# Kernel tuning notes

Hardware: AMD Instinct MI355X
Metric: run time of the kernel (lower is better)

Reference implementation:

```python
import jax, jax.numpy as jnp
import numpy as np

# NTU RGB+D 25-joint skeleton edges (1-based)
NTU_EDGES = [(1,2),(2,21),(3,21),(4,3),(5,21),(6,5),(7,6),(8,7),(9,21),(10,9),
             (11,10),(12,11),(13,1),(14,13),(15,14),(16,15),(17,1),(18,17),
             (19,18),(20,19),(22,23),(23,8),(24,25),(25,12)]
NUM_SCALES = 13
NUM_POINT = 25


def build_A_powers(num_scales=NUM_SCALES, v=NUM_POINT):
    # MS-G3D disentangled multi-scale aggregation: exact-k-hop adjacencies, each
    # with self loops, symmetrically normalized, stacked along dim 0 -> (K*V, V).
    A = np.zeros((v, v))
    for i, j in NTU_EDGES:
        A[i - 1, j - 1] = 1.0
        A[j - 1, i - 1] = 1.0
    I = np.eye(v)
    mats = []
    for k in range(num_scales):
        if k == 0:
            Ak = I.copy()
        else:
            Ak = np.minimum(np.linalg.matrix_power(A + I, k), 1) \
               - np.minimum(np.linalg.matrix_power(A + I, k - 1), 1)
            Ak = Ak + I  # with_self=True
        d = Ak.sum(-1)
        dinv = np.where(d > 0, d ** -0.5, 0.0)
        mats.append((dinv[:, None] * Ak) * dinv[None, :])
    return np.concatenate(mats, 0).astype(np.float32)


def batchnorm(x, g, b, axes, ch_axis, eps=1e-5):
    # torch BatchNorm in training mode: biased batch stats + affine
    mean = jnp.mean(x, axes, keepdims=True)
    var = jnp.mean((x - mean) ** 2, axes, keepdims=True)
    shape = [1] * x.ndim
    shape[ch_axis] = -1
    return (x - mean) * jax.lax.rsqrt(var + eps) * g.reshape(shape) + b.reshape(shape)


def ms_gcn(x, A_powers, A_res, W, b, g, beta, num_scales):
    # x: (N, C, T, V); A: (K*V, V)
    A = A_powers + A_res
    support = jnp.einsum('vu,nctu->nctv', A, x)            # (N, C, T, K*V)
    N, C, T, KV = support.shape
    V = KV // num_scales
    support = support.reshape(N, C, T, num_scales, V).transpose(0, 3, 1, 2, 4)
    support = support.reshape(N, num_scales * C, T, V)     # (N, K*C, T, V)
    out = jnp.einsum('oc,nctv->notv', W, support) + b[None, :, None, None]  # 1x1 conv
    out = batchnorm(out, g, beta, (0, 2, 3), 1)
    return jax.nn.relu(out)


def lstm(x, Wih, Whh, bih, bhh):
    # single-layer batch_first LSTM, zero initial state; torch gate order i,f,g,o
    B = x.shape[0]
    H = Whh.shape[1]
    xp = jnp.einsum('bsd,hd->bsh', x, Wih) + bih + bhh     # precompute input proj

    def step(carry, xt):
        h, c = carry
        gates = xt + h @ Whh.T
        i, f, g, o = jnp.split(gates, 4, axis=-1)
        c = jax.nn.sigmoid(f) * c + jax.nn.sigmoid(i) * jnp.tanh(g)
        h = jax.nn.sigmoid(o) * jnp.tanh(c)
        return (h, c), h

    init = (jnp.zeros((B, H), x.dtype), jnp.zeros((B, H), x.dtype))
    _, ys = jax.lax.scan(step, init, jnp.swapaxes(xp, 0, 1))
    return jnp.swapaxes(ys, 0, 1)                          # (B, S, H)


def logsig_rnn(x, n_segments, Wih, Whh, bih, bhh):
    # x: (B, T, d). Depth-2 log-signature per time segment + segment start point,
    # concatenated and fed to an LSTM (Logsig-RNN layer).
    B, T, d = x.shape
    t_vec = np.array([int(round(float(v))) for v in np.linspace(1, T, n_segments + 1)])
    starts = t_vec[:-1] - 1
    ends = t_vec[1:] - 1
    L = int((ends - starts).max()) + 1
    # pad segments to fixed length by repeating the last point (zero increments)
    idx = np.minimum(starts[:, None] + np.arange(L)[None, :], ends[:, None])  # (S, L)
    pts = x[:, idx, :]                                     # (B, S, L, d)
    rel = pts - pts[:, :, :1, :]
    inc = rel[:, :, -1, :]                                 # level-1: total increment
    dx = pts[:, :, 1:, :] - pts[:, :, :-1, :]
    Mm = jnp.einsum('bsli,bslj->bsij', rel[:, :, :-1, :], dx)
    iu, ju = np.triu_indices(d, k=1)
    levy = 0.5 * (Mm[:, :, iu, ju] - Mm[:, :, ju, iu])     # level-2 (Lyndon basis)
    feats = jnp.concatenate([x[:, starts, :], inc, levy], axis=-1)
    return lstm(feats, Wih, Whh, bih, bhh)


def setup_inputs() -> dict:
    key = jax.random.key(0)
    ks = iter(jax.random.split(key, 16))
    N, C, T, V, M = 2, 3, 100, 25, 2
    c1, c2, num_class, K = 96, 192, 60, NUM_SCALES

    def randn(shape, scale):
        return jax.random.normal(next(ks), shape, jnp.float32) * scale

    ls1 = c1 + c1 * (c1 - 1) // 2     # 4656
    ls2 = c2 + c2 * (c2 - 1) // 2     # 18528
    in1 = c1 + ls1                    # 4752
    in2 = c2 + ls2                    # 18720
    Ap = jnp.asarray(build_A_powers())
    return {
        'x': jax.random.normal(next(ks), (N, C, T, V, M), jnp.float32),
        'length': jax.random.randint(next(ks), (N,), 0, T),
        'data_bn_g': jnp.ones((M * V * C,)), 'data_bn_b': jnp.zeros((M * V * C,)),
        'A_powers1': Ap,
        'A_res1': jax.random.uniform(next(ks), Ap.shape, jnp.float32, -1e-6, 1e-6),
        'W1': randn((c1, K * C), (K * C) ** -0.5), 'b1': jnp.zeros((c1,)),
        'bn1_g': jnp.ones((c1,)), 'bn1_b': jnp.zeros((c1,)),
        'Wih1': randn((4 * c1, in1), in1 ** -0.5), 'Whh1': randn((4 * c1, c1), c1 ** -0.5),
        'bih1': jnp.zeros((4 * c1,)), 'bhh1': jnp.zeros((4 * c1,)),
        'bnseg1_g': jnp.ones((50,)), 'bnseg1_b': jnp.zeros((50,)),
        'A_powers2': Ap,
        'A_res2': jax.random.uniform(next(ks), Ap.shape, jnp.float32, -1e-6, 1e-6),
        'W2': randn((c2, K * c1), (K * c1) ** -0.5), 'b2': jnp.zeros((c2,)),
        'bn2_g': jnp.ones((c2,)), 'bn2_b': jnp.zeros((c2,)),
        'Wih2': randn((4 * c2, in2), in2 ** -0.5), 'Whh2': randn((4 * c2, c2), c2 ** -0.5),
        'bih2': jnp.zeros((4 * c2,)), 'bhh2': jnp.zeros((4 * c2,)),
        'bnseg2_g': jnp.ones((30,)), 'bnseg2_b': jnp.zeros((30,)),
        'fcW': randn((num_class, c2), c2 ** -0.5), 'fcb': jnp.zeros((num_class,)),
    }


def reference(x, length, data_bn_g, data_bn_b, A_powers1, A_res1, W1, b1, bn1_g, bn1_b,
              Wih1, Whh1, bih1, bhh1, bnseg1_g, bnseg1_b, A_powers2, A_res2, W2, b2,
              bn2_g, bn2_b, Wih2, Whh2, bih2, bhh2, bnseg2_g, bnseg2_b, fcW, fcb):
    # `length` is accepted but unused, as in the original forward.
    N, C, T, V, M = x.shape
    K = A_powers1.shape[0] // V
    c1, c2 = W1.shape[0], W2.shape[0]
    S1, S2 = 50, 30

    h = x.transpose(0, 4, 3, 1, 2).reshape(N, M * V * C, T)
    h = batchnorm(h, data_bn_g, data_bn_b, (0, 2), 1)
    h = h.reshape(N * M, V, C, T).transpose(0, 2, 3, 1)            # (NM, C, T, V)

    h = jax.nn.relu(ms_gcn(h, A_powers1, A_res1, W1, b1, bn1_g, bn1_b, K))
    h = h.transpose(0, 3, 2, 1).reshape(N * M * V, T, c1)
    h = logsig_rnn(h, S1, Wih1, Whh1, bih1, bhh1)                  # (NMV, S1, c1)
    h = batchnorm(h, bnseg1_g, bnseg1_b, (0, 2), 1)
    h = h.reshape(N * M, V, S1, c1).transpose(0, 3, 2, 1)          # (NM, c1, S1, V)

    h = jax.nn.relu(ms_gcn(h, A_powers2, A_res2, W2, b2, bn2_g, bn2_b, K))
    h = h.transpose(0, 3, 2, 1).reshape(N * M * V, S1, c2)
    h = logsig_rnn(h, S2, Wih2, Whh2, bih2, bhh2)                  # (NMV, S2, c2)
    h = batchnorm(h, bnseg2_g, bnseg2_b, (0, 2), 1)
    h = h.reshape(N * M, V, S2, c2).transpose(0, 3, 2, 1)          # (NM, c2, S2, V)

    pooled = h.reshape(N, M, c2, -1).mean(axis=3).mean(axis=1)     # (N, c2)
    return pooled @ fcW.T + fcb
```

## Files before the change

kernel.cpp:

```cpp
#include <hip/hip_runtime.h>
#include <cmath>
#include <cstdint>
#include <cstddef>

typedef unsigned short bf16_t;
typedef __attribute__((ext_vector_type(8))) short short8;
typedef __attribute__((ext_vector_type(4))) float floatx4;
typedef __attribute__((ext_vector_type(2))) _Float16 half2_t;

__device__ __forceinline__ float bf2f(bf16_t b){
  unsigned int u = ((unsigned int)b) << 16;
  return __uint_as_float(u);
}
__device__ __forceinline__ bf16_t f2bf(float f){
  unsigned int u = __float_as_uint(f);
  unsigned int r = (u + 0x7fffu + ((u >> 16) & 1u)) >> 16;
  return (bf16_t)r;
}
__device__ __forceinline__ unsigned int f2bf2(float a, float b){
  return (unsigned int)f2bf(a) | ((unsigned int)f2bf(b) << 16);
}
__device__ __forceinline__ float sigf(float x){ return 1.0f / (1.0f + expf(-x)); }

__device__ __forceinline__ float dot2(half2_t a, half2_t b, float c){
#if __has_builtin(__builtin_amdgcn_fdot2)
  return __builtin_amdgcn_fdot2(a, b, c, false);
#else
  return c + (float)a.x * (float)b.x + (float)a.y * (float)b.y;
#endif
}

__device__ __forceinline__ void gload_lds16(const bf16_t* g, bf16_t* lds){
  __builtin_amdgcn_global_load_lds(
      (const __attribute__((address_space(1))) unsigned int*)g,
      (__attribute__((address_space(3))) unsigned int*)lds, 16, 0, 0);
}

__device__ __forceinline__ void barrier_raw(){
  asm volatile("s_barrier" ::: "memory");
}

__device__ __forceinline__ int xcd_chunk_swizzle(int orig, int nwg){
  int q = nwg >> 3, r = nwg & 7;
  int xcd = orig & 7, idx = orig >> 3;
  return (xcd < r ? xcd * (q + 1) : r * (q + 1) + (xcd - r) * q) + idx;
}

__global__ void prep_misc(const float* __restrict__ a1, const float* __restrict__ r1, float* __restrict__ o1,
                          const float* __restrict__ a2, const float* __restrict__ r2, float* __restrict__ o2,
                          const float* __restrict__ bi1, const float* __restrict__ bh1, float* __restrict__ ob1,
                          const float* __restrict__ bi2, const float* __restrict__ bh2, float* __restrict__ ob2,
                          const float* __restrict__ Whh1, half2_t* __restrict__ Wp1,
                          const float* __restrict__ Whh2, half2_t* __restrict__ Wp2,
                          unsigned short* __restrict__ lut1, unsigned short* __restrict__ lut2,
                          float* __restrict__ stats, bf16_t* __restrict__ A2mat){
  int i = blockIdx.x * blockDim.x + threadIdx.x;
  if (i < 8125){ o1[i] = a1[i] + r1[i]; o2[i] = a2[i] + r2[i]; }
  if (i < 384) ob1[i] = bi1[i] + bh1[i];
  if (i < 768) ob2[i] = bi2[i] + bh2[i];
  if (i < 736) stats[i] = 0.f;
  if (i < 18432){
    int t = i % 384, j2 = i / 384;
    half2_t w; w.x = (_Float16)Whh1[(size_t)t * 96 + 2 * j2];
    w.y = (_Float16)Whh1[(size_t)t * 96 + 2 * j2 + 1];
    Wp1[i] = w;
  }
  if (i < 73728){
    int t = i % 768, j2 = i / 768;
    half2_t w; w.x = (_Float16)Whh2[(size_t)t * 192 + 2 * j2];
    w.y = (_Float16)Whh2[(size_t)t * 192 + 2 * j2 + 1];
    Wp2[i] = w;
  }
  if (i < 4560){
    int d = 96, p = i;
    int r = (int)(((2.0 * d - 1.0) - sqrt((2.0 * d - 1.0) * (2.0 * d - 1.0) - 8.0 * (double)p)) * 0.5);
    if (r < 0) r = 0;
    while (r + 1 <= d - 2 && (r + 1) * (d - 1) - ((r + 1) * r) / 2 <= p) ++r;
    while (r > 0 && r * (d - 1) - (r * (r - 1)) / 2 > p) --r;
    int jj = p - (r * (d - 1) - (r * (r - 1)) / 2);
    lut1[p] = (unsigned short)((r << 8) | (r + 1 + jj));
  }
  if (i < 18336){
    int d = 192, p = i;
    int r = (int)(((2.0 * d - 1.0) - sqrt((2.0 * d - 1.0) * (2.0 * d - 1.0) - 8.0 * (double)p)) * 0.5);
    if (r < 0) r = 0;
    while (r + 1 <= d - 2 && (r + 1) * (d - 1) - ((r + 1) * r) / 2 <= p) ++r;
    while (r > 0 && r * (d - 1) - (r * (r - 1)) / 2 > p) --r;
    int jj = p - (r * (d - 1) - (r * (r - 1)) / 2);
    lut2[p] = (unsigned short)((r << 8) | (r + 1 + jj));
  }
  if (i < 160000){
    int row = i >> 5, col = 1248 + (i & 31);
    A2mat[(size_t)row * 1280 + col] = 0;
  }
}

__device__ __forceinline__ void f2bf_seg(const float* in, bf16_t* out, int Kin, int Kout, int li){
  int ko8 = Kout >> 3;
  int r = li / ko8, k8 = (li % ko8) << 3;
  uint4 u;
  if (k8 + 8 <= Kin){
    const float4* p = reinterpret_cast<const float4*>(in + (size_t)r * Kin + k8);
    float4 x0 = p[0], x1 = p[1];
    u.x = f2bf2(x0.x, x0.y); u.y = f2bf2(x0.z, x0.w);
    u.z = f2bf2(x1.x, x1.y); u.w = f2bf2(x1.z, x1.w);
  } else {
    u.x = u.y = u.z = u.w = 0u;
  }
  *reinterpret_cast<uint4*>(out + (size_t)r * Kout + k8) = u;
}

__global__ void f2bf_pad8_3(const float* __restrict__ in1, bf16_t* __restrict__ out1, int Kin1, int Kout1, int c1,
                            const float* __restrict__ in2, bf16_t* __restrict__ out2, int Kin2, int Kout2, int c2,
                            const float* __restrict__ in3, bf16_t* __restrict__ out3, int Kin3, int Kout3, int c3){
  int idx = blockIdx.x * blockDim.x + threadIdx.x;
  if (idx < c1){ f2bf_seg(in1, out1, Kin1, Kout1, idx); return; }
  idx -= c1;
  if (idx < c2){ f2bf_seg(in2, out2, Kin2, Kout2, idx); return; }
  idx -= c2;
  if (idx < c3) f2bf_seg(in3, out3, Kin3, Kout3, idx);
}

__global__ void data_bn_kernel(const float* __restrict__ x, const float* __restrict__ g,
                               const float* __restrict__ bb, float* __restrict__ h1,
                               int N, int C, int T, int V, int M){
  int ch = blockIdx.x;
  int m = ch / (V * C);
  int v = (ch / C) % V;
  int c = ch % C;
  int tid = threadIdx.x;
  int cnt = N * T;
  float s = 0.f, s2 = 0.f;
  for (int i = tid; i < cnt; i += 64){
    int n = i / T, t = i % T;
    float val = x[(((size_t)(n * C + c) * T + t) * V + v) * M + m];
    s += val; s2 += val * val;
  }
  for (int off = 32; off; off >>= 1){ s += __shfl_down(s, off); s2 += __shfl_down(s2, off); }
  s = __shfl(s, 0); s2 = __shfl(s2, 0);
  float mean = s / cnt;
  float rstd = rsqrtf(s2 / cnt - mean * mean + 1e-5f);
  float gg = g[ch], bo = bb[ch];
  for (int i = tid; i < cnt; i += 64){
    int n = i / T, t = i % T;
    float val = x[(((size_t)(n * C + c) * T + t) * V + v) * M + m];
    float y = (val - mean) * rstd * gg + bo;
    h1[((size_t)((n * M + m) * C + c) * T + t) * V + v] = y;
  }
}

__global__ __launch_bounds__(256)
void gcn1_fused(const float* __restrict__ A, const float* __restrict__ h1,
                const float* __restrict__ W1, const float* __restrict__ b1,
                float* __restrict__ y1, float* __restrict__ ssum, float* __restrict__ ssq, int T){
  __shared__ float h[3][25];
  __shared__ float sup[3][325];
  __shared__ float lsum[96], lsq[96];
  int blk = blockIdx.x;
  int nm = blk / T, t = blk % T;
  int tid = threadIdx.x;
  if (tid < 75){
    int c = tid / 25, v = tid % 25;
    h[c][v] = h1[((size_t)(nm * 3 + c) * T + t) * 25 + v];
  }
  if (tid < 96){ lsum[tid] = 0.f; lsq[tid] = 0.f; }
  __syncthreads();
  for (int w = tid; w < 975; w += 256){
    int c = w / 325, ww = w % 325;
    const float* ar = A + ww * 25;
    float acc = 0.f;
    #pragma unroll
    for (int u = 0; u < 25; ++u) acc += ar[u] * h[c][u];
    sup[c][ww] = acc;
  }
  __syncthreads();
  for (int o2 = tid; o2 < 2400; o2 += 256){
    int v = o2 / 96, o = o2 % 96;
    float acc = b1[o];
    #pragma unroll
    for (int k = 0; k < 13; ++k)
      #pragma unroll
      for (int c = 0; c < 3; ++c)
        acc += W1[o * 39 + k * 3 + c] * sup[c][k * 25 + v];
    y1[((size_t)blk * 25 + v) * 96 + o] = acc;
    atomicAdd(&lsum[o], acc);
    atomicAdd(&lsq[o], acc * acc);
  }
  __syncthreads();
  if (tid < 96){ atomicAdd(&ssum[tid], lsum[tid]); atomicAdd(&ssq[tid], lsq[tid]); }
}

struct SegTable { int st[50]; int en[50]; };

__global__ void feats_bn_kernel(const float* __restrict__ ymat, const float* __restrict__ sum,
                                const float* __restrict__ sumsq, const float* __restrict__ g,
                                const float* __restrict__ bb, bf16_t* __restrict__ feats,
                                SegTable segs, const unsigned int* __restrict__ lut32,
                                int T, int d, int S, int L, int pairs, int rowlenP, int R){
  __shared__ float pts[4][192];
  int bs = blockIdx.x;
  int b = bs / S, s = bs % S;
  int nm = b / 25, v = b % 25;
  int st = segs.st[s], en = segs.en[s];
  int nt = blockDim.x, tid = threadIdx.x;
  for (int l = 0; l < L; ++l){
    int t = st + l; if (t > en) t = en;
    const float* yrow = ymat + ((size_t)(nm * T + t) * 25 + v) * d;
    for (int i = tid; i < d; i += nt){
      float mean = sum[i] / R;
      float rstd = rsqrtf(sumsq[i] / R - mean * mean + 1e-5f);
      pts[l][i] = fmaxf((yrow[i] - mean) * rstd * g[i] + bb[i], 0.f);
    }
  }
  __syncthreads();
  unsigned int* frow32 = reinterpret_cast<unsigned int*>(feats + (size_t)bs * rowlenP);
  int d2 = d >> 1;
  for (int i2 = tid; i2 < d2; i2 += nt){
    int i = 2 * i2;
    frow32[i2]      = f2bf2(pts[0][i], pts[0][i + 1]);
    frow32[d2 + i2] = f2bf2(pts[L - 1][i] - pts[0][i], pts[L - 1][i + 1] - pts[0][i + 1]);
  }
  int rowlen2 = (2 * d + pairs) >> 1, rowlenP2 = rowlenP >> 1;
  for (int i = tid + rowlen2; i < rowlenP2; i += nt) frow32[i] = 0;
  int Lm2 = L - 2;
  unsigned int* lrow32 = frow32 + d;
  int pairs2 = pairs >> 1;
  for (int p2 = tid; p2 < pairs2; p2 += nt){
    unsigned int ee = lut32[p2];
    int i0 = (ee >> 8) & 255, j0 = ee & 255;
    int i1 = ee >> 24, j1 = (ee >> 16) & 255;
    float acc0 = 0.f, acc1 = 0.f;
    for (int l = 1; l <= Lm2; ++l){
      float ri = pts[l][i0] - pts[0][i0], rj = pts[l][j0] - pts[0][j0];
      float di = pts[l + 1][i0] - pts[l][i0], dj = pts[l + 1][j0] - pts[l][j0];
      acc0 += ri * dj - rj * di;
      float ri1 = pts[l][i1] - pts[0][i1], rj1 = pts[l][j1] - pts[0][j1];
      float di1 = pts[l + 1][i1] - pts[l][i1], dj1 = pts[l + 1][j1] - pts[l][j1];
      acc1 += ri1 * dj1 - rj1 * di1;
    }
    lrow32[p2] = f2bf2(0.5f * acc0, 0.5f * acc1);
  }
}

__global__ __launch_bounds__(256)
void gemm_mfma_nt_split(const bf16_t* __restrict__ A, const bf16_t* __restrict__ B,
                        float* __restrict__ P, int M, int N, int K,
                        int GX, int GY, int GZ){
  __shared__ bf16_t As[128 * 64];
  __shared__ bf16_t Bs[128 * 64];
  const int nwg = GX * GY * GZ;
  const int wg = xcd_chunk_swizzle(blockIdx.x, nwg);
  const int bxi = wg % GX, byi = (wg / GX) % GY, bzi = wg / (GX * GY);
  const int tid = threadIdx.x;
  const int lane = tid & 63, wv = tid >> 6;
  const int bm = bxi * 128, bn = byi * 128;
  const int wr = (wv >> 1) * 64, wc = (wv & 1) * 64;
  const int m_l = lane & 15, q = lane >> 4;

  const int ksteps = K >> 6;
  const int Z = GZ, z = bzi;
  const int per = (ksteps + Z - 1) / Z;
  const int ks0 = z * per;
  const int ks1 = (ks0 + per < ksteps) ? ks0 + per : ksteps;

  const int rlane = lane >> 3;
  const int slane = lane & 7;
  const int colc = (slane ^ rlane) * 8;
  const bf16_t* gA[4]; const bf16_t* gB[4];
  bf16_t* lA[4]; bf16_t* lB[4];
  #pragma unroll
  for (int it = 0; it < 4; ++it){
    int c = it * 4 + wv;
    int rowA = bm + c * 8 + rlane; if (rowA > M - 1) rowA = M - 1;
    int rowB = bn + c * 8 + rlane; if (rowB > N - 1) rowB = N - 1;
    gA[it] = A + (size_t)rowA * K + colc;
    gB[it] = B + (size_t)rowB * K + colc;
    lA[it] = &As[c * 512];
    lB[it] = &Bs[c * 512];
  }
  const int sxor = m_l & 7;

  floatx4 acc[4][4] = {};
  for (int ks = ks0; ks < ks1; ++ks){
    int k0 = ks << 6;
    __syncthreads();
    #pragma unroll
    for (int it = 0; it < 4; ++it){
      gload_lds16(gA[it] + k0, lA[it]);
      gload_lds16(gB[it] + k0, lB[it]);
    }
    __syncthreads();
    #pragma unroll
    for (int half = 0; half < 2; ++half){
      const int scol = ((half * 4 + q) ^ sxor) * 8;
      short8 af[4], bfr[4];
      #pragma unroll
      for (int i = 0; i < 4; ++i){
        af[i]  = *reinterpret_cast<const short8*>(&As[(wr + i * 16 + m_l) * 64 + scol]);
        bfr[i] = *reinterpret_cast<const short8*>(&Bs[(wc + i * 16 + m_l) * 64 + scol]);
      }
      #pragma unroll
      for (int mi = 0; mi < 4; ++mi)
        #pragma unroll
        for (int ni = 0; ni < 4; ++ni)
          acc[mi][ni] = __builtin_amdgcn_mfma_f32_16x16x32_bf16(af[mi], bfr[ni], acc[mi][ni], 0, 0, 0);
    }
  }

  float* Pz = P + (size_t)z * M * N;
  #pragma unroll
  for (int mi = 0; mi < 4; ++mi){
    int row0 = bm + wr + mi * 16 + q * 4;
    #pragma unroll
    for (int r = 0; r < 4; ++r){
      int row = row0 + r;
      if (row < M){
        #pragma unroll
        for (int ni = 0; ni < 4; ++ni){
          int col = bn + wc + ni * 16 + m_l;
          if (col < N) Pz[(size_t)row * N + col] = acc[mi][ni][r];
        }
      }
    }
  }
}

#define VMC4 asm volatile("s_waitcnt vmcnt(4)" ::: "memory")
#define VMC0 asm volatile("s_waitcnt vmcnt(0)" ::: "memory")
#define STG_A8(NB, KH, OFF) { gload_lds16(pA0 + (OFF) + (KH) * 32, dA0 + (NB) * 16384 + (KH) * 8192); \
                              gload_lds16(pA1 + (OFF) + (KH) * 32, dA1 + (NB) * 16384 + (KH) * 8192); }
#define STG_B8(NB, KH, OFF) { gload_lds16(pB0 + (OFF) + (KH) * 32, dB0 + (NB) * 16384 + (KH) * 8192); \
                              gload_lds16(pB1 + (OFF) + (KH) * 32, dB1 + (NB) * 16384 + (KH) * 8192); }
#define PH8(BUF, KH, MIB, LOADB, STAGE_BLOCK, WAIT_BLOCK) { \
    const bf16_t* ab_ = As + (BUF) * 16384 + (KH) * 8192 + sA + (MIB) * 512; \
    _Pragma("unroll") \
    for (int i_ = 0; i_ < 4; ++i_) af[i_] = *reinterpret_cast<const short8*>(ab_ + i_ * 512); \
    if (LOADB){ \
      const bf16_t* bb_ = Bs + (BUF) * 16384 + (KH) * 8192 + sB; \
      _Pragma("unroll") \
      for (int i_ = 0; i_ < 4; ++i_) bfr[i_] = *reinterpret_cast<const short8*>(bb_ + i_ * 512); \
    } \
    STAGE_BLOCK; \
    WAIT_BLOCK; \
    barrier_raw(); \
    __builtin_amdgcn_s_setprio(1); \
    _Pragma("unroll") \
    for (int mi_ = 0; mi_ < 4; ++mi_) \
      _Pragma("unroll") \
      for (int ni_ = 0; ni_ < 4; ++ni_) \
        acc[(MIB) + mi_][ni_] = __builtin_amdgcn_mfma_f32_16x16x32_bf16(af[mi_], bfr[ni_], acc[(MIB) + mi_][ni_], 0, 0, 0); \
    __builtin_amdgcn_s_setprio(0); \
  }

__global__ __launch_bounds__(512, 2)
void gemm_mfma_nt_8ph(const bf16_t* __restrict__ A, const bf16_t* __restrict__ B,
                      float* __restrict__ P, int M, int N, int K,
                      int GX, int GY, int GZ){
  __shared__ bf16_t As[32768];
  __shared__ bf16_t Bs[32768];
  const int nwg = GX * GY * GZ;
  const int wg = xcd_chunk_swizzle(blockIdx.x, nwg);
  const int bxi = wg % GX, byi = (wg / GX) % GY, bzi = wg / (GX * GY);
  const int tid = threadIdx.x;
  const int lane = tid & 63, wv = tid >> 6;
  const int wm = wv >> 2, wn = wv & 3;
  const int m_l = lane & 15, q = lane >> 4;
  const int bm = bxi * 256, bn = byi * 256;

  const int ksteps = K >> 6;
  const int z = bzi, Z = GZ;
  const int per = (ksteps + Z - 1) / Z;
  const int ks0 = z * per;
  int ks1 = ks0 + per; if (ks1 > ksteps) ks1 = ksteps;
  if (ks0 >= ks1) return;

  const int rlane = lane >> 2, slane = lane & 3;
  const int cg = slane ^ ((rlane >> 1) & 3);
  int rr0 = wv * 16 + rlane, rr1 = (8 + wv) * 16 + rlane;
  int ra0 = bm + rr0; if (ra0 > M - 1) ra0 = M - 1;
  int ra1 = bm + rr1; if (ra1 > M - 1) ra1 = M - 1;
  int rb0 = bn + rr0; if (rb0 > N - 1) rb0 = N - 1;
  int rb1 = bn + rr1; if (rb1 > N - 1) rb1 = N - 1;
  const bf16_t* pA0 = A + (size_t)ra0 * K + cg * 8 + ks0 * 64;
  const bf16_t* pA1 = A + (size_t)ra1 * K + cg * 8 + ks0 * 64;
  const bf16_t* pB0 = B + (size_t)rb0 * K + cg * 8 + ks0 * 64;
  const bf16_t* pB1 = B + (size_t)rb1 * K + cg * 8 + ks0 * 64;
  bf16_t* dA0 = As + wv * 512;
  bf16_t* dA1 = As + (8 + wv) * 512;
  bf16_t* dB0 = Bs + wv * 512;
  bf16_t* dB1 = Bs + (8 + wv) * 512;

  const int sA = (wm * 128 + m_l) * 32 + ((q ^ ((m_l >> 1) & 3)) * 8);
  const int sB = (wn * 64 + m_l) * 32 + ((q ^ ((m_l >> 1) & 3)) * 8);

  short8 af[4], bfr[4];
  floatx4 acc[8][4] = {};

  STG_A8(0, 0, 0); STG_B8(0, 0, 0); STG_A8(0, 1, 0); STG_B8(0, 1, 0);
  VMC4;
  barrier_raw();

  int buf = 0;
  for (int t = ks0; t < ks1 - 1; ++t){
    const int nb = buf ^ 1;
    PH8(buf, 0, 0, true,  STG_A8(nb, 0, 64), ((void)0));
    PH8(buf, 0, 4, false, STG_B8(nb, 0, 64), VMC4);
    PH8(buf, 1, 0, true,  STG_A8(nb, 1, 64), ((void)0));
    PH8(buf, 1, 4, false, STG_B8(nb, 1, 64), VMC4);
    pA0 += 64; pA1 += 64; pB0 += 64; pB1 += 64;
    buf = nb;
  }
  PH8(buf, 0, 0, true,  ((void)0), ((void)0));
  PH8(buf, 0, 4, false, ((void)0), VMC0);
  PH8(buf, 1, 0, true,  ((void)0), ((void)0));
  PH8(buf, 1, 4, false, ((void)0), ((void)0));

  float* Pz = P + (size_t)z * M * N;
  #pragma unroll
  for (int mi = 0; mi < 8; ++mi){
    int row0 = bm + wm * 128 + mi * 16 + q * 4;
    #pragma unroll
    for (int r = 0; r < 4; ++r){
      int row = row0 + r;
      if (row < M){
        #pragma unroll
        for (int ni = 0; ni < 4; ++ni){
          int col = bn + wn * 64 + ni * 16 + m_l;
          if (col < N) Pz[(size_t)row * N + col] = acc[mi][ni][r];
        }
      }
    }
  }
}

__global__ __launch_bounds__(256)
void reduce_split_bias_stats(const float* __restrict__ P, const float* __restrict__ bias,
                             float* __restrict__ out, float* __restrict__ ssum, float* __restrict__ ssq,
                             int MN, int N, int Z){
  __shared__ float lsum[192], lsq[192];
  int tid = threadIdx.x;
  if (tid < 192){ lsum[tid] = 0.f; lsq[tid] = 0.f; }
  __syncthreads();
  int i4 = (blockIdx.x * blockDim.x + tid) * 4;
  if (i4 < MN){
    const float4 bv = *reinterpret_cast<const float4*>(bias + (i4 % N));
    float4 s = bv;
    for (int z = 0; z < Z; ++z){
      const float4 p = *reinterpret_cast<const float4*>(P + (size_t)z * MN + i4);
      s.x += p.x; s.y += p.y; s.z += p.z; s.w += p.w;
    }
    *reinterpret_cast<float4*>(out + i4) = s;
    int c0 = i4 % N;
    atomicAdd(&lsum[c0],     s.x); atomicAdd(&lsq[c0],     s.x * s.x);
    atomicAdd(&lsum[c0 + 1], s.y); atomicAdd(&lsq[c0 + 1], s.y * s.y);
    atomicAdd(&lsum[c0 + 2], s.z); atomicAdd(&lsq[c0 + 2], s.z * s.z);
    atomicAdd(&lsum[c0 + 3], s.w); atomicAdd(&lsq[c0 + 3], s.w * s.w);
  }
  __syncthreads();
  if (tid < 192){ atomicAdd(&ssum[tid], lsum[tid]); atomicAdd(&ssq[tid], lsq[tid]); }
}

template <int H2C, int BLK, int Z>
__global__ __launch_bounds__(BLK)
void lstm_kernel(const float* __restrict__ P, const float* __restrict__ bias,
                 const half2_t* __restrict__ Wp, float* __restrict__ out,
                 float* __restrict__ ssum, float* __restrict__ ssq,
                 int S, int MN){
  constexpr int H = 2 * H2C;
  constexpr int H4 = 4 * H;
  __shared__ _Float16 __attribute__((aligned(16))) hsh[H];
  __shared__ float gv[H4];
  __shared__ float ra[BLK / 64], rb[BLK / 64];
  const int b = blockIdx.x, t = threadIdx.x;
  const int lane = t & 63, wid = t >> 6;
  half2_t w[H2C];
  const half2_t* wp = Wp + t;
  #pragma unroll
  for (int j2 = 0; j2 < H2C; ++j2) w[j2] = wp[(size_t)j2 * H4];
  float cc = 0.f;
  if (t < H) hsh[t] = (_Float16)0.f;
  const float bval = bias[t];
  const size_t base = (size_t)b * S * H4 + t;
  float pv0[Z], pv1[Z];
  #pragma unroll
  for (int z = 0; z < Z; ++z) pv0[z] = P[(size_t)z * MN + base];
  #pragma unroll
  for (int z = 0; z < Z; ++z) pv1[z] = P[(size_t)z * MN + base + H4];
  __syncthreads();
  const half2_t* hp = reinterpret_cast<const half2_t*>(hsh);
  for (int s = 0; s < S; ++s){
    float pvn[Z];
    if (s + 2 < S){
      size_t o2 = base + (size_t)(s + 2) * H4;
      #pragma unroll
      for (int z = 0; z < Z; ++z) pvn[z] = P[(size_t)z * MN + o2];
    }
    float a0 = bval, a1 = 0.f, a2 = 0.f, a3 = 0.f;
    float a4 = 0.f, a5 = 0.f, a6 = 0.f, a7 = 0.f;
    #pragma unroll
    for (int z = 0; z < Z; ++z) a0 += pv0[z];
    #pragma unroll
    for (int j2 = 0; j2 < H2C; j2 += 8){
      a0 = dot2(w[j2],     hp[j2],     a0);
      a1 = dot2(w[j2 + 1], hp[j2 + 1], a1);
      a2 = dot2(w[j2 + 2], hp[j2 + 2], a2);
      a3 = dot2(w[j2 + 3], hp[j2 + 3], a3);
      a4 = dot2(w[j2 + 4], hp[j2 + 4], a4);
      a5 = dot2(w[j2 + 5], hp[j2 + 5], a5);
      a6 = dot2(w[j2 + 6], hp[j2 + 6], a6);
      a7 = dot2(w[j2 + 7], hp[j2 + 7], a7);
    }
    gv[t] = ((a0 + a1) + (a2 + a3)) + ((a4 + a5) + (a6 + a7));
    __syncthreads();
    float gvv = 0.f;
    if (t < H){
      float ig = sigf(gv[t]);
      float fg = sigf(gv[H + t]);
      float gg = tanhf(gv[2 * H + t]);
      float og = sigf(gv[3 * H + t]);
      cc = fg * cc + ig * gg;
      float hh = og * tanhf(cc);
      hsh[t] = (_Float16)hh;
      out[((size_t)b * S + s) * H + t] = hh;
      gvv = hh;
    }
    float q1 = gvv, q2 = gvv * gvv;
    for (int off2 = 32; off2; off2 >>= 1){ q1 += __shfl_down(q1, off2); q2 += __shfl_down(q2, off2); }
    if (lane == 0){ ra[wid] = q1; rb[wid] = q2; }
    __syncthreads();
    if (t == 0){
      float sa = 0.f, sb = 0.f;
      #pragma unroll
      for (int ww = 0; ww < BLK / 64; ++ww){ sa += ra[ww]; sb += rb[ww]; }
      atomicAdd(&ssum[s], sa);
      atomicAdd(&ssq[s], sb);
    }
    #pragma unroll
    for (int z = 0; z < Z; ++z){ pv0[z] = pv1[z]; pv1[z] = pvn[z]; }
  }
}

__global__ void support2_bn(const float* __restrict__ A, const float* __restrict__ lout,
                            const float* __restrict__ ssum, const float* __restrict__ ssq,
                            const float* __restrict__ g, const float* __restrict__ bb,
                            bf16_t* __restrict__ A2mat, int S, int cnt){
  int idx = blockIdx.x * blockDim.x + threadIdx.x;
  int total = 4 * S * 25 * 13 * 96;
  if (idx >= total) return;
  int c = idx % 96;
  int k = (idx / 96) % 13;
  int v = (idx / (96 * 13)) % 25;
  int rs = idx / (96 * 13 * 25);
  int s = rs % S, nm = rs / S;
  float mean = ssum[s] / cnt;
  float rstd = rsqrtf(ssq[s] / cnt - mean * mean + 1e-5f);
  float scale = rstd * g[s];
  float shift = bb[s] - mean * scale;
  const float* ar = A + (k * 25 + v) * 25;
  float acc = 0.f;
  #pragma unroll
  for (int u = 0; u < 25; ++u){
    float raw = lout[((size_t)(nm * 25 + u) * S + s) * 96 + c];
    acc += ar[u] * (raw * scale + shift);
  }
  A2mat[((size_t)rs * 25 + v) * 1280 + k * 96 + c] = f2bf(acc);
}

__global__ void pool_kernel(const float* __restrict__ lout2, const float* __restrict__ sum,
                            const float* __restrict__ sumsq, const float* __restrict__ g,
                            const float* __restrict__ bb, float* __restrict__ pooled,
                            int S, int H, int scnt){
  int n = blockIdx.x / H;
  int o = blockIdx.x % H;
  float acc = 0.f;
  int cnt = 2 * 25 * S;
  for (int i = threadIdx.x; i < cnt; i += 64){
    int m = i / (25 * S);
    int r = i % (25 * S);
    int v = r / S;
    int s = r % S;
    int b = (n * 2 + m) * 25 + v;
    float val = lout2[((size_t)b * S + s) * H + o];
    float mean = sum[s] / scnt;
    float rstd = rsqrtf(sumsq[s] / scnt - mean * mean + 1e-5f);
    val = (val - mean) * rstd * g[s] + bb[s];
    acc += val;
  }
  for (int off = 32; off; off >>= 1) acc += __shfl_down(acc, off);
  if (threadIdx.x == 0) pooled[n * H + o] = acc / cnt;
}

__global__ void fc_kernel(const float* __restrict__ pooled, const float* __restrict__ fcW,
                          const float* __restrict__ fcb, float* __restrict__ outp){
  int idx = blockIdx.x * blockDim.x + threadIdx.x;
  if (idx >= 120) return;
  int n = idx / 60, cls = idx % 60;
  float acc = fcb[cls];
  for (int o = 0; o < 192; ++o) acc += pooled[n * 192 + o] * fcW[cls * 192 + o];
  outp[idx] = acc;
}

static void make_segs(int T, int S, SegTable& tab, int& L){
  double step = (double)(T - 1) / (double)S;
  long long tv[51];
  for (int i = 0; i <= S; ++i){
    double v = 1.0 + step * (double)i;
    tv[i] = llrint(v);
  }
  L = 0;
  for (int s = 0; s < S; ++s){
    tab.st[s] = (int)tv[s] - 1;
    tab.en[s] = (int)tv[s + 1] - 1;
    int len = tab.en[s] - tab.st[s] + 1;
    if (len > L) L = len;
  }
  for (int s = S; s < 50; ++s){ tab.st[s] = 0; tab.en[s] = 0; }
  if (L > 4) L = 4;
}

extern "C" void kernel_launch(void* const* d_in, const int* in_sizes, int n_in,
                              void* d_out, int out_size, void* d_ws, size_t ws_size,
                              hipStream_t stream){
  const float* x         = (const float*)d_in[0];
  const float* data_bn_g = (const float*)d_in[2];
  const float* data_bn_b = (const float*)d_in[3];
  const float* A_powers1 = (const float*)d_in[4];
  const float* A_res1    = (const float*)d_in[5];
  const float* W1        = (const float*)d_in[6];
  const float* b1        = (const float*)d_in[7];
  const float* bn1_g     = (const float*)d_in[8];
  const float* bn1_b     = (const float*)d_in[9];
  const float* Wih1      = (const float*)d_in[10];
  const float* Whh1      = (const float*)d_in[11];
  const float* bih1      = (const float*)d_in[12];
  const float* bhh1      = (const float*)d_in[13];
  const float* bnseg1_g  = (const float*)d_in[14];
  const float* bnseg1_b  = (const float*)d_in[15];
  const float* A_powers2 = (const float*)d_in[16];
  const float* A_res2    = (const float*)d_in[17];
  const float* W2        = (const float*)d_in[18];
  const float* b2        = (const float*)d_in[19];
  const float* bn2_g     = (const float*)d_in[20];
  const float* bn2_b     = (const float*)d_in[21];
  const float* Wih2      = (const float*)d_in[22];
  const float* Whh2      = (const float*)d_in[23];
  const float* bih2      = (const float*)d_in[24];
  const float* bhh2      = (const float*)d_in[25];
  const float* bnseg2_g  = (const float*)d_in[26];
  const float* bnseg2_b  = (const float*)d_in[27];
  const float* fcW       = (const float*)d_in[28];
  const float* fcb       = (const float*)d_in[29];
  float* out = (float*)d_out;

  const int N = 2, C = 3, T = 100, V = 25, M = 2, NM = 4;
  const int C1 = 96, C2 = 192;
  const int S1 = 50, S2 = 30;
  const int B = 100;
  const int IN1 = 4752, IN2 = 18720;
  const int IN1P = 4800, IN2P = 18752;
  const int P1 = 4560, P2 = 18336;
  const int KG2 = 1248, KG2P = 1280;
  const int Z1 = 5, Z2 = 7, ZG = 4;

  size_t off = 0;
  char* base = (char*)d_ws;
  auto alloc = [&](size_t nbytes) -> void* {
    off = (off + 255) & ~(size_t)255;
    void* p = base + off;
    off += nbytes;
    return p;
  };
  float* A1full = (float*)alloc(325 * 25 * 4);
  float* A2full = (float*)alloc(325 * 25 * 4);
  float* h1     = (float*)alloc((size_t)NM * C * T * V * 4);
  float* y1mat  = (float*)alloc((size_t)NM * T * V * C1 * 4);
  float* stats  = (float*)alloc(736 * 4);
  float* st1a = stats, *st1b = stats + 96;
  float* sg1a = stats + 192, *sg1b = stats + 242;
  float* st2a = stats + 292, *st2b = stats + 484;
  float* sg2a = stats + 676, *sg2b = stats + 706;
  float* l1out  = (float*)alloc((size_t)B * S1 * C1 * 4);
  bf16_t* A2mat = (bf16_t*)alloc((size_t)NM * S1 * V * KG2P * 2);
  float* y2mat  = (float*)alloc((size_t)NM * S1 * V * C2 * 4);
  float* l2out  = (float*)alloc((size_t)B * S2 * C2 * 4);
  float* pooled = (float*)alloc(2 * C2 * 4);
  float* bias1  = (float*)alloc(4 * C1 * 4);
  float* bias2  = (float*)alloc(4 * C2 * 4);
  half2_t* Wp1  = (half2_t*)alloc((size_t)(C1 / 2) * 4 * C1 * 4);
  half2_t* Wp2  = (half2_t*)alloc((size_t)(C2 / 2) * 4 * C2 * 4);
  bf16_t* Wih1b = (bf16_t*)alloc((size_t)4 * C1 * IN1P * 2);
  bf16_t* Wih2b = (bf16_t*)alloc((size_t)4 * C2 * IN2P * 2);
  bf16_t* W2b   = (bf16_t*)alloc((size_t)C2 * KG2P * 2);
  unsigned short* lut1 = (unsigned short*)alloc((size_t)P1 * 2);
  unsigned short* lut2 = (unsigned short*)alloc((size_t)P2 * 2);
  size_t pmax = (size_t)Z2 * 3000 * 768;
  {
    size_t p1s = (size_t)Z1 * 5000 * 384; if (p1s > pmax) pmax = p1s;
    size_t pgs = (size_t)ZG * 5000 * 192; if (pgs > pmax) pmax = pgs;
  }
  float* Pbuf = (float*)alloc(pmax * 4);
  bf16_t* feats = (bf16_t*)alloc((size_t)B * S2 * IN2P * 2);
  (void)ws_size; (void)in_sizes; (void)n_in; (void)out_size;

  prep_misc<<<625, 256, 0, stream>>>(A_powers1, A_res1, A1full, A_powers2, A_res2, A2full,
                                     bih1, bhh1, bias1, bih2, bhh2, bias2,
                                     Whh1, Wp1, Whh2, Wp2, lut1, lut2, stats, A2mat);
  {
    int c1 = 4 * C1 * (IN1P / 8);
    int c2 = 4 * C2 * (IN2P / 8);
    int c3 = C2 * (KG2P / 8);
    int tot = c1 + c2 + c3;
    f2bf_pad8_3<<<(tot + 255) / 256, 256, 0, stream>>>(Wih1, Wih1b, IN1, IN1P, c1,
                                                       Wih2, Wih2b, IN2, IN2P, c2,
                                                       W2, W2b, KG2, KG2P, c3);
  }

  data_bn_kernel<<<M * V * C, 64, 0, stream>>>(x, data_bn_g, data_bn_b, h1, N, C, T, V, M);

  gcn1_fused<<<NM * T, 256, 0, stream>>>(A1full, h1, W1, b1, y1mat, st1a, st1b, T);

  SegTable seg1, seg2; int L1, L2;
  make_segs(T, S1, seg1, L1);
  make_segs(S1, S2, seg2, L2);

  feats_bn_kernel<<<B * S1, 256, 0, stream>>>(y1mat, st1a, st1b, bn1_g, bn1_b, feats, seg1,
                                              (const unsigned int*)lut1, T, C1, S1, L1, P1, IN1P,
                                              NM * T * 25);
  {
    int Mm = B * S1, Nn = 4 * C1;
    int GX = (Mm + 127) / 128, GY = (Nn + 127) / 128;
    gemm_mfma_nt_split<<<GX * GY * Z1, 256, 0, stream>>>(feats, Wih1b, Pbuf, Mm, Nn, IN1P,
                                                         GX, GY, Z1);
    lstm_kernel<48, 384, Z1><<<B, 384, 0, stream>>>(Pbuf, bias1, Wp1, l1out, sg1a, sg1b, S1, Mm * Nn);
  }

  {
    int tot = NM * S1 * 25 * 13 * 96;
    support2_bn<<<(tot + 255) / 256, 256, 0, stream>>>(A2full, l1out, sg1a, sg1b, bnseg1_g,
                                                       bnseg1_b, A2mat, S1, B * C1);
  }
  {
    int Mm = NM * S1 * 25, Nn = C2;
    int GX = (Mm + 127) / 128, GY = (Nn + 127) / 128;
    gemm_mfma_nt_split<<<GX * GY * ZG, 256, 0, stream>>>(A2mat, W2b, Pbuf, Mm, Nn, KG2P,
                                                         GX, GY, ZG);
    int MN = Mm * Nn;
    reduce_split_bias_stats<<<(MN / 4 + 255) / 256, 256, 0, stream>>>(Pbuf, b2, y2mat, st2a, st2b,
                                                                      MN, Nn, ZG);
  }

  feats_bn_kernel<<<B * S2, 256, 0, stream>>>(y2mat, st2a, st2b, bn2_g, bn2_b, feats, seg2,
                                              (const unsigned int*)lut2, S1, C2, S2, L2, P2, IN2P,
                                              NM * S1 * 25);
  {
    int Mm = B * S2, Nn = 4 * C2;
    int GX = (Mm + 255) / 256, GY = (Nn + 255) / 256;
    gemm_mfma_nt_8ph<<<GX * GY * Z2, 512, 0, stream>>>(feats, Wih2b, Pbuf, Mm, Nn, IN2P,
                                                       GX, GY, Z2);
    lstm_kernel<96, 768, Z2><<<B, 768, 0, stream>>>(Pbuf, bias2, Wp2, l2out, sg2a, sg2b, S2, Mm * Nn);
  }

  pool_kernel<<<2 * C2, 64, 0, stream>>>(l2out, sg2a, sg2b, bnseg2_g, bnseg2_b, pooled, S2, C2, B * C2);
  fc_kernel<<<1, 128, 0, stream>>>(pooled, fcW, fcb, out);
}
```

Before: 659.2 us.

## Restructure 8-phase GEMM into 2 half-phases and use it for layer-1 LSTM projection

The 256x256 MFMA GEMM kernel drops from four sub-phases per k-step to two. Each phase now loads all 8 A fragments plus the B fragments, issues all four staging loads, and runs 32 MFMAs between barriers, which halves barrier count but raises register pressure. The layer-1 input-projection GEMM now uses this 512-thread 256x256 tiled kernel in place of the 128x128 split kernel, with split-K raised from 5 to 6 to keep enough workgroups. Larger tiles cut redundant global loads but leave fewer blocks, with partial edge tiles on the 384-wide N dimension.

```diff
diff --git a/kernel.cpp b/kernel.cpp
--- a/kernel.cpp
+++ b/kernel.cpp
@@ -327,28 +327,26 @@
 
 #define VMC4 asm volatile("s_waitcnt vmcnt(4)" ::: "memory")
 #define VMC0 asm volatile("s_waitcnt vmcnt(0)" ::: "memory")
-#define STG_A8(NB, KH, OFF) { gload_lds16(pA0 + (OFF) + (KH) * 32, dA0 + (NB) * 16384 + (KH) * 8192); \
-                              gload_lds16(pA1 + (OFF) + (KH) * 32, dA1 + (NB) * 16384 + (KH) * 8192); }
-#define STG_B8(NB, KH, OFF) { gload_lds16(pB0 + (OFF) + (KH) * 32, dB0 + (NB) * 16384 + (KH) * 8192); \
-                              gload_lds16(pB1 + (OFF) + (KH) * 32, dB1 + (NB) * 16384 + (KH) * 8192); }
-#define PH8(BUF, KH, MIB, LOADB, STAGE_BLOCK, WAIT_BLOCK) { \
-    const bf16_t* ab_ = As + (BUF) * 16384 + (KH) * 8192 + sA + (MIB) * 512; \
+#define STG4(NB, KH, OFF) { gload_lds16(pA0 + (OFF) + (KH) * 32, dA0 + (NB) * 16384 + (KH) * 8192); \
+                            gload_lds16(pA1 + (OFF) + (KH) * 32, dA1 + (NB) * 16384 + (KH) * 8192); \
+                            gload_lds16(pB0 + (OFF) + (KH) * 32, dB0 + (NB) * 16384 + (KH) * 8192); \
+                            gload_lds16(pB1 + (OFF) + (KH) * 32, dB1 + (NB) * 16384 + (KH) * 8192); }
+#define HP(BUF, KH, STAGE_BLOCK, WAIT_BLOCK) { \
+    const bf16_t* ab_ = As + (BUF) * 16384 + (KH) * 8192 + sA; \
     _Pragma("unroll") \
-    for (int i_ = 0; i_ < 4; ++i_) af[i_] = *reinterpret_cast<const short8*>(ab_ + i_ * 512); \
-    if (LOADB){ \
-      const bf16_t* bb_ = Bs + (BUF) * 16384 + (KH) * 8192 + sB; \
-      _Pragma("unroll") \
-      for (int i_ = 0; i_ < 4; ++i_) bfr[i_] = *reinterpret_cast<const short8*>(bb_ + i_ * 512); \
-    } \
+    for (int i_ = 0; i_ < 8; ++i_) af[i_] = *reinterpret_cast<const short8*>(ab_ + i_ * 512); \
+    const bf16_t* bb_ = Bs + (BUF) * 16384 + (KH) * 8192 + sB; \
+    _Pragma("unroll") \
+    for (int i_ = 0; i_ < 4; ++i_) bfr[i_] = *reinterpret_cast<const short8*>(bb_ + i_ * 512); \
     STAGE_BLOCK; \
     WAIT_BLOCK; \
     barrier_raw(); \
     __builtin_amdgcn_s_setprio(1); \
     _Pragma("unroll") \
-    for (int mi_ = 0; mi_ < 4; ++mi_) \
+    for (int mi_ = 0; mi_ < 8; ++mi_) \
       _Pragma("unroll") \
       for (int ni_ = 0; ni_ < 4; ++ni_) \
-        acc[(MIB) + mi_][ni_] = __builtin_amdgcn_mfma_f32_16x16x32_bf16(af[mi_], bfr[ni_], acc[(MIB) + mi_][ni_], 0, 0, 0); \
+        acc[mi_][ni_] = __builtin_amdgcn_mfma_f32_16x16x32_bf16(af[mi_], bfr[ni_], acc[mi_][ni_], 0, 0, 0); \
     __builtin_amdgcn_s_setprio(0); \
   }
 
@@ -393,27 +391,23 @@
   const int sA = (wm * 128 + m_l) * 32 + ((q ^ ((m_l >> 1) & 3)) * 8);
   const int sB = (wn * 64 + m_l) * 32 + ((q ^ ((m_l >> 1) & 3)) * 8);
 
-  short8 af[4], bfr[4];
+  short8 af[8], bfr[4];
   floatx4 acc[8][4] = {};
 
-  STG_A8(0, 0, 0); STG_B8(0, 0, 0); STG_A8(0, 1, 0); STG_B8(0, 1, 0);
+  STG4(0, 0, 0); STG4(0, 1, 0);
   VMC4;
   barrier_raw();
 
   int buf = 0;
   for (int t = ks0; t < ks1 - 1; ++t){
     const int nb = buf ^ 1;
-    PH8(buf, 0, 0, true,  STG_A8(nb, 0, 64), ((void)0));
-    PH8(buf, 0, 4, false, STG_B8(nb, 0, 64), VMC4);
-    PH8(buf, 1, 0, true,  STG_A8(nb, 1, 64), ((void)0));
-    PH8(buf, 1, 4, false, STG_B8(nb, 1, 64), VMC4);
+    HP(buf, 0, STG4(nb, 0, 64), VMC4);
+    HP(buf, 1, STG4(nb, 1, 64), VMC4);
     pA0 += 64; pA1 += 64; pB0 += 64; pB1 += 64;
     buf = nb;
   }
-  PH8(buf, 0, 0, true,  ((void)0), ((void)0));
-  PH8(buf, 0, 4, false, ((void)0), VMC0);
-  PH8(buf, 1, 0, true,  ((void)0), ((void)0));
-  PH8(buf, 1, 4, false, ((void)0), ((void)0));
+  HP(buf, 0, ((void)0), VMC0);
+  HP(buf, 1, ((void)0), ((void)0));
 
   float* Pz = P + (size_t)z * M * N;
   #pragma unroll
@@ -660,7 +654,7 @@
   const int IN1P = 4800, IN2P = 18752;
   const int P1 = 4560, P2 = 18336;
   const int KG2 = 1248, KG2P = 1280;
-  const int Z1 = 5, Z2 = 7, ZG = 4;
+  const int Z1 = 6, Z2 = 7, ZG = 4;
 
   size_t off = 0;
   char* base = (char*)d_ws;
@@ -728,9 +722,9 @@
                                               NM * T * 25);
   {
     int Mm = B * S1, Nn = 4 * C1;
-    int GX = (Mm + 127) / 128, GY = (Nn + 127) / 128;
-    gemm_mfma_nt_split<<<GX * GY * Z1, 256, 0, stream>>>(feats, Wih1b, Pbuf, Mm, Nn, IN1P,
-                                                         GX, GY, Z1);
+    int GX = (Mm + 255) / 256, GY = (Nn + 255) / 256;
+    gemm_mfma_nt_8ph<<<GX * GY * Z1, 512, 0, stream>>>(feats, Wih1b, Pbuf, Mm, Nn, IN1P,
+                                                       GX, GY, Z1);
     lstm_kernel<48, 384, Z1><<<B, 384, 0, stream>>>(Pbuf, bias1, Wp1, l1out, sg1a, sg1b, S1, Mm * Nn);
   }
 
```

After: 622.6 us. -5.5%, faster.
